# Optimization experiments

Hardware: AMD Instinct MI355X
Metric: run time of the kernel (lower is better)

The kernel has to match this reference:

```python
import jax, jax.numpy as jnp
import numpy as np

V, E, U = 32000, 256, 512  # vocab, embed dim, LSTM units
B, S = 16, 130             # batch, seq len


def lstm_layer(x, mask, k, r, b):
    """Keras LSTMCell semantics. x:[B,T,D], mask:[B,T]; gates order i,f,c,o."""
    h0 = jnp.zeros((x.shape[0], U), x.dtype)
    c0 = h0
    xs = jnp.swapaxes(x, 0, 1)      # [T,B,D]
    ms = jnp.swapaxes(mask, 0, 1)   # [T,B]

    def step(carry, inp):
        h, c = carry
        xt, mt = inp
        z = xt @ k + h @ r + b
        i, f, g, o = jnp.split(z, 4, axis=-1)
        i = jax.nn.sigmoid(i); f = jax.nn.sigmoid(f); o = jax.nn.sigmoid(o)
        cn = f * c + i * jnp.tanh(g)
        hn = o * jnp.tanh(cn)
        m = mt[:, None]
        hn = jnp.where(m, hn, h)  # masked steps carry previous state/output
        cn = jnp.where(m, cn, c)
        return (hn, cn), hn

    _, ys = jax.lax.scan(step, (h0, c0), (xs, ms))
    return jnp.swapaxes(ys, 0, 1)  # [B,T,U]


def stacked_lstm(x, mask, params):
    h = x
    for (k, r, b) in params:
        h = lstm_layer(h, mask, k, r, b)
    return h


def setup_inputs() -> dict:
    key = jax.random.key(0)
    ks = jax.random.split(key, 20)
    d = {}
    d["seqs"] = jax.random.randint(ks[0], (B, S), 0, V)
    d["emb"] = jax.random.normal(ks[1], (V, E), jnp.float32) * 0.01
    i = 2
    for pre in ("f", "b"):
        in_dims = [E, U]
        for l in range(2):
            d[f"{pre}k{l}"] = jax.random.normal(ks[i], (in_dims[l], 4 * U), jnp.float32) * 0.05; i += 1
            d[f"{pre}r{l}"] = jax.random.normal(ks[i], (U, 4 * U), jnp.float32) * 0.05; i += 1
            d[f"{pre}b{l}"] = jnp.zeros((4 * U,), jnp.float32)
    d["Wp"] = jax.random.normal(ks[i], (2 * U, V), jnp.float32) * 0.02
    d["bp"] = jnp.zeros((V,), jnp.float32)
    return d


def reference(seqs, emb, fk0, fr0, fb0, fk1, fr1, fb1, bk0, br0, bb0, bk1, br1, bb1, Wp, bp):
    mask = seqs != 0                 # mask_zero=True
    embedded = emb[seqs]             # [B,S,E]
    # forward LM over tokens 0..S-2
    f = stacked_lstm(embedded[:, :-1], mask[:, :-1], [(fk0, fr0, fb0), (fk1, fr1, fb1)])
    # backward LM over tokens 1..S-1 (go_backwards: scan reversed input)
    xb = embedded[:, 1:][:, ::-1]
    mb = mask[:, 1:][:, ::-1]
    b = stacked_lstm(xb, mb, [(bk0, br0, bb0), (bk1, br1, bb1)])
    b_rev = b[:, ::-1]               # tf.reverse -> chronological order
    o = jnp.concatenate([f[:, :-1], b_rev[:, 1:]], axis=-1)  # [B,S-2,2U]
    return o @ Wp + bp               # [B,S-2,V]
```

## Files before the change

### kernel.cpp

```cpp
#include <hip/hip_runtime.h>

typedef __attribute__((ext_vector_type(8))) short bf16x8;
typedef __attribute__((ext_vector_type(4))) float f32x4;

__device__ __forceinline__ unsigned short f2bf(float x){
  union { float f; unsigned u; } v; v.f = x;
  unsigned r = v.u + 0x7FFFu + ((v.u >> 16) & 1u);
  return (unsigned short)(r >> 16);
}

__device__ __forceinline__ float sigm(float x){
  return 1.f / (1.f + __builtin_amdgcn_exp2f(-1.44269504f * x));
}
__device__ __forceinline__ float tanhfast(float x){
  return 2.f / (1.f + __builtin_amdgcn_exp2f(-2.88539008f * x)) - 1.f;
}

#define BYPASS_ST_SHORT(base, val) \
  asm volatile("global_store_short %0, %1, off sc0 sc1" :: "v"(base), "v"(val))

__device__ __forceinline__ int ld_flag(const int* p){
  int v;
  asm volatile("global_load_dword %0, %1, off sc0 sc1\n\t"
               "s_waitcnt vmcnt(0)"
               : "=v"(v) : "v"(p) : "memory");
  return v;
}

__device__ __forceinline__ void gload_lds16(const void* g, void* l){
  __builtin_amdgcn_global_load_lds(
      (const __attribute__((address_space(1))) unsigned*)g,
      (__attribute__((address_space(3))) unsigned*)l, 16, 0, 0);
}

__global__ void embed_kernel(const int* __restrict__ seqs, const float* __restrict__ emb,
                             unsigned short* __restrict__ x, int* __restrict__ mask,
                             int* __restrict__ flags){
  const int t = blockIdx.x, b = blockIdx.y, l = threadIdx.x;
  if (t == 0 && b == 0){
    #pragma unroll
    for (int j = 0; j < 16; ++j) flags[l + j*64] = 0;
  }
  const int tok = seqs[b*130 + t];
  if (l == 0) mask[b*130 + t] = (tok != 0) ? 1 : 0;
  const float* src = emb + (size_t)tok * 256;
  unsigned short* dst = x + ((size_t)b*130 + t)*256;
  #pragma unroll
  for (int j = 0; j < 4; ++j) dst[l + j*64] = f2bf(src[l + j*64]);
}

__global__ __launch_bounds__(512) void prep_small(
    const float* __restrict__ fk0, unsigned short* __restrict__ fk0T,
    const float* __restrict__ fr0, unsigned short* __restrict__ fr0T,
    const float* __restrict__ fk1, unsigned short* __restrict__ fk1T,
    const float* __restrict__ fr1, unsigned short* __restrict__ fr1T,
    const float* __restrict__ bk0, unsigned short* __restrict__ bk0T,
    const float* __restrict__ br0, unsigned short* __restrict__ br0T,
    const float* __restrict__ bk1, unsigned short* __restrict__ bk1T,
    const float* __restrict__ br1, unsigned short* __restrict__ br1T)
{
  __shared__ float tf[32*65];
  const int tid = threadIdx.x;
  const int tx = tid & 63, ty = tid >> 6;
  const int orow = tid & 31, oc = tid >> 5;
  for (int tile = blockIdx.x; tile < 3584; tile += gridDim.x){
    const float* src; unsigned short* dst; int R, r0, c0;
    int u = tile;
    if (u < 256)      { src = fk0; dst = fk0T; R = 256;           }
    else if (u < 768) { src = fr0; dst = fr0T; R = 512; u -= 256; }
    else if (u < 1280){ src = fk1; dst = fk1T; R = 512; u -= 768; }
    else if (u < 1792){ src = fr1; dst = fr1T; R = 512; u -= 1280;}
    else if (u < 2048){ src = bk0; dst = bk0T; R = 256; u -= 1792;}
    else if (u < 2560){ src = br0; dst = br0T; R = 512; u -= 2048;}
    else if (u < 3072){ src = bk1; dst = bk1T; R = 512; u -= 2560;}
    else              { src = br1; dst = br1T; R = 512; u -= 3072;}
    const int kt = u >> 5, nt = u & 31;
    r0 = kt*32; c0 = nt*64;
    #pragma unroll
    for (int j = 0; j < 4; ++j)
      tf[(ty + 8*j)*65 + tx] = src[(size_t)(r0 + ty + 8*j)*2048 + c0 + tx];
    __syncthreads();
    #pragma unroll
    for (int j = 0; j < 4; ++j)
      dst[(size_t)(c0 + oc + 16*j)*R + r0 + orow] = f2bf(tf[orow*65 + oc + 16*j]);
    __syncthreads();
  }
}

__global__ __launch_bounds__(512, 2) void lstm_coop(
    const unsigned short* __restrict__ x, const int* __restrict__ maskg,
    const unsigned short* __restrict__ fk0T, const unsigned short* __restrict__ fr0T,
    const unsigned short* __restrict__ fk1T, const unsigned short* __restrict__ fr1T,
    const unsigned short* __restrict__ bk0T, const unsigned short* __restrict__ br0T,
    const unsigned short* __restrict__ bk1T, const unsigned short* __restrict__ br1T,
    const float* __restrict__ fb0, const float* __restrict__ fb1,
    const float* __restrict__ bb0, const float* __restrict__ bb1,
    const float* __restrict__ Wp, unsigned short* __restrict__ WpT,
    unsigned short* h0f, unsigned short* h0b,
    unsigned short* aproj, int* flags)
{
  const int wg = blockIdx.x;
  const int tid = threadIdx.x;

  __shared__ float z_lds[4][16][32];
  __shared__ int mask_s[16*130];
  __shared__ __attribute__((aligned(16))) char h_lds[16*1024];
  __shared__ __attribute__((aligned(16))) char h2_lds[16*1024];

  if (wg >= 64){
    float* tf = (float*)h_lds;
    const int tw = wg - 64;
    const int tx = tid & 63, ty = tid >> 6;
    const int orow = tid & 31, oc = tid >> 5;
    for (int tile = tw; tile < 16000; tile += 96){
      const int kt = tile / 500, nt = tile - kt*500;
      const int r0 = kt*32, c0 = nt*64;
      #pragma unroll
      for (int j = 0; j < 4; ++j)
        tf[(ty + 8*j)*65 + tx] = Wp[(size_t)(r0 + ty + 8*j)*32000 + c0 + tx];
      __syncthreads();
      #pragma unroll
      for (int j = 0; j < 4; ++j)
        WpT[(size_t)(c0 + oc + 16*j)*1024 + r0 + orow] = f2bf(tf[orow*65 + oc + 16*j]);
      __syncthreads();
    }
    return;
  }

  const int dir = wg >> 5;
  const int layer = (wg >> 4) & 1;
  const int u0 = (wg & 15) * 32;
  const int w = tid >> 6, l = tid & 63;
  const int gate = w >> 1, half = w & 1;
  const int lr = l & 15, lk = l >> 4;
  const int cglob = gate*512 + u0 + half*16 + lr;

  const unsigned short* kT = (layer == 0) ? (dir ? bk0T : fk0T) : (dir ? bk1T : fk1T);
  const unsigned short* rT = (layer == 0) ? (dir ? br0T : fr0T) : (dir ? br1T : fr1T);
  const float* bias = (layer == 0) ? (dir ? bb0 : fb0) : (dir ? bb1 : fb1);
  unsigned short* h0 = dir ? h0b : h0f;

  int* fown  = flags + (layer*2 + dir)*256;
  int* fprod = flags + dir*256;
  int* fself = fown + (wg & 15)*16;

  bf16x8 wreg[16], kreg[16];
  #pragma unroll
  for (int i = 0; i < 16; ++i)
    wreg[i] = *(const bf16x8*)(rT + (size_t)cglob*512 + i*32 + lk*8);
  if (layer == 0){
    #pragma unroll
    for (int i = 0; i < 8; ++i)
      kreg[i] = *(const bf16x8*)(kT + (size_t)cglob*256 + i*32 + lk*8);
  } else {
    #pragma unroll
    for (int i = 0; i < 16; ++i)
      kreg[i] = *(const bf16x8*)(kT + (size_t)cglob*512 + i*32 + lk*8);
  }

  for (int i = tid; i < 16*130; i += 512) mask_s[i] = maskg[i];

  float c_reg = 0.f, h_reg = 0.f;
  const int gu = tid & 31, gb = tid >> 5;
  const float bzi = bias[u0+gu], bzf = bias[512 + u0+gu];
  const float bzc = bias[1024 + u0+gu], bzo = bias[1536 + u0+gu];
  __syncthreads();

  for (int t = 0; t < 128; ++t){
    {
      const int* fp = nullptr; int tgt = 0;
      if (l < 16){ fp = fown + l*16; tgt = t; }
      else if (l < 32 && layer == 1){ fp = fprod + (l-16)*16; tgt = t + 1; }
      if (fp){
        while (ld_flag(fp) < tgt) __builtin_amdgcn_s_sleep(1);
      }
    }

    const int r0s = w*2;
    if (layer == 0){
      if (t > 0){
        #pragma unroll
        for (int j = 0; j < 2; ++j){
          const int r = r0s + j;
          const unsigned short* g = h0 + ((size_t)(t-1)*16 + r)*512 + ((l ^ (r & 7))*8);
          gload_lds16(g, h_lds + r*1024);
        }
      }
    } else {
      #pragma unroll
      for (int j = 0; j < 2; ++j){
        const int r = r0s + j;
        const unsigned short* g = h0 + ((size_t)t*16 + r)*512 + ((l ^ (r & 7))*8);
        gload_lds16(g, h_lds + r*1024);
      }
      if (t > 0){
        const int prow = dir ? (128 - t) : (t - 1);
        #pragma unroll
        for (int j = 0; j < 2; ++j){
          const int r = r0s + j;
          const unsigned short* g = aproj + ((size_t)(r*128 + prow))*1024 + dir*512 + ((l ^ (r & 7))*8);
          gload_lds16(g, h2_lds + r*1024);
        }
      }
    }

    f32x4 a0 = {0.f,0.f,0.f,0.f}, a1 = a0;
    const int fsw = (lr & 7) << 4;
    if (layer == 0){
      const int pos = dir ? (129 - t) : t;
      const unsigned short* xa = x + ((size_t)lr*130 + pos)*256 + lk*8;
      #pragma unroll
      for (int i = 0; i < 8; i += 2){
        bf16x8 va = *(const bf16x8*)(xa + i*32);
        bf16x8 vb = *(const bf16x8*)(xa + i*32 + 32);
        a0 = __builtin_amdgcn_mfma_f32_16x16x32_bf16(va, kreg[i],   a0, 0, 0, 0);
        a1 = __builtin_amdgcn_mfma_f32_16x16x32_bf16(vb, kreg[i+1], a1, 0, 0, 0);
      }
      if (t > 0){
        asm volatile("s_waitcnt vmcnt(0)" ::: "memory");
        __syncthreads();
        #pragma unroll
        for (int i = 0; i < 16; i += 2){
          bf16x8 v0 = *(const bf16x8*)(h_lds + lr*1024 + ((lk*16 + (i  )*64) ^ fsw));
          bf16x8 v1 = *(const bf16x8*)(h_lds + lr*1024 + ((lk*16 + (i+1)*64) ^ fsw));
          a0 = __builtin_amdgcn_mfma_f32_16x16x32_bf16(v0, wreg[i],   a0, 0, 0, 0);
          a1 = __builtin_amdgcn_mfma_f32_16x16x32_bf16(v1, wreg[i+1], a1, 0, 0, 0);
        }
      }
    } else {
      asm volatile("s_waitcnt vmcnt(0)" ::: "memory");
      __syncthreads();
      #pragma unroll
      for (int i = 0; i < 16; i += 2){
        bf16x8 v0 = *(const bf16x8*)(h_lds + lr*1024 + ((lk*16 + (i  )*64) ^ fsw));
        bf16x8 v1 = *(const bf16x8*)(h_lds + lr*1024 + ((lk*16 + (i+1)*64) ^ fsw));
        a0 = __builtin_amdgcn_mfma_f32_16x16x32_bf16(v0, kreg[i],   a0, 0, 0, 0);
        a1 = __builtin_amdgcn_mfma_f32_16x16x32_bf16(v1, kreg[i+1], a1, 0, 0, 0);
      }
      if (t > 0){
        #pragma unroll
        for (int i = 0; i < 16; i += 2){
          bf16x8 v0 = *(const bf16x8*)(h2_lds + lr*1024 + ((lk*16 + (i  )*64) ^ fsw));
          bf16x8 v1 = *(const bf16x8*)(h2_lds + lr*1024 + ((lk*16 + (i+1)*64) ^ fsw));
          a0 = __builtin_amdgcn_mfma_f32_16x16x32_bf16(v0, wreg[i],   a0, 0, 0, 0);
          a1 = __builtin_amdgcn_mfma_f32_16x16x32_bf16(v1, wreg[i+1], a1, 0, 0, 0);
        }
      }
    }
    {
      f32x4 acc = a0 + a1;
      #pragma unroll
      for (int r = 0; r < 4; ++r) z_lds[gate][lk*4 + r][half*16 + lr] = acc[r];
    }
    __syncthreads();

    {
      const float zi = z_lds[0][gb][gu] + bzi;
      const float zf = z_lds[1][gb][gu] + bzf;
      const float zc = z_lds[2][gb][gu] + bzc;
      const float zo = z_lds[3][gb][gu] + bzo;
      const float iv = sigm(zi);
      const float fv = sigm(zf);
      const float ov = sigm(zo);
      const float gv = tanhfast(zc);
      float cn = fv*c_reg + iv*gv;
      float hn = ov*tanhfast(cn);
      const int pos = dir ? (129 - t) : t;
      if (mask_s[gb*130 + pos] == 0){ cn = c_reg; hn = h_reg; }
      c_reg = cn; h_reg = hn;
      const unsigned short hb = f2bf(hn);
      if (layer == 0){
        unsigned short* p = h0 + ((size_t)t*16 + gb)*512 + u0 + gu;
        BYPASS_ST_SHORT(p, (unsigned)hb);
      } else {
        const int row = dir ? (127 - t) : t;
        unsigned short* p = aproj + ((size_t)gb*128 + row)*1024 + dir*512 + u0 + gu;
        BYPASS_ST_SHORT(p, (unsigned)hb);
      }
    }
    asm volatile("s_waitcnt vmcnt(0)" ::: "memory");
    __syncthreads();
    if (tid == 0){
      int v = t + 1;
      asm volatile("global_store_dword %0, %1, off sc0 sc1" :: "v"(fself), "v"(v) : "memory");
    }
  }
}

__global__ __launch_bounds__(256) void gemm_bf16(
    const unsigned short* __restrict__ A, const unsigned short* __restrict__ Bt,
    const float* __restrict__ bias, float* __restrict__ C,
    int M, int N, int K)
{
  __shared__ unsigned short lA[3][128*32], lB[3][128*32];
  const int tid = threadIdx.x;
  const int w = tid >> 6, l = tid & 63;
  const int wr = w >> 1, wc = w & 1;
  const int lr = l & 15, lk = l >> 4;
  const int orig = blockIdx.x;
  const int logical = (orig & 7)*500 + (orig >> 3);
  const int mt = logical & 15;
  const int nt = logical >> 4;
  const int brow = mt * 128, bcol = nt * 128;

  const int base0 = w*2048;
  const int base1 = w*2048 + 1024;
  const int L0 = base0 + l*16, L1 = base1 + l*16;
  const int Lg0 = L0 ^ (((L0 >> 7) & 3) << 4);
  const int Lg1 = L1 ^ (((L1 >> 7) & 3) << 4);
  const int row0 = Lg0 >> 6, kb0 = Lg0 & 63;
  const int row1 = Lg1 >> 6, kb1 = Lg1 & 63;

  f32x4 acc[4][4] = {};

  #define STAGE_KT(kt_, bu_) do{ \
    const int k0_ = (kt_) * 32; \
    gload_lds16((const char*)(A + (size_t)(brow+row0)*K + k0_) + kb0, (char*)lA[bu_] + base0); \
    gload_lds16((const char*)(Bt + (size_t)(bcol+row0)*K + k0_) + kb0, (char*)lB[bu_] + base0); \
    gload_lds16((const char*)(A + (size_t)(brow+row1)*K + k0_) + kb1, (char*)lA[bu_] + base1); \
    gload_lds16((const char*)(Bt + (size_t)(bcol+row1)*K + k0_) + kb1, (char*)lB[bu_] + base1); \
  }while(0)

  STAGE_KT(0, 0);
  STAGE_KT(1, 1);
  asm volatile("s_waitcnt vmcnt(4)" ::: "memory");
  __syncthreads();

  for (int kt = 0; kt < 32; ++kt){
    const int bu = kt - (kt / 3) * 3;
    if (kt < 30){
      const int nb = (kt + 2) - ((kt + 2) / 3) * 3;
      STAGE_KT(kt + 2, nb);
    }
    bf16x8 af[4], bfr[4];
    #pragma unroll
    for (int m = 0; m < 4; ++m){
      const int L = (wr*64 + m*16 + lr)*64 + lk*16;
      const int sp = L ^ (((L >> 7) & 3) << 4);
      af[m] = *(const bf16x8*)((char*)lA[bu] + sp);
    }
    #pragma unroll
    for (int n = 0; n < 4; ++n){
      const int L = (wc*64 + n*16 + lr)*64 + lk*16;
      const int sp = L ^ (((L >> 7) & 3) << 4);
      bfr[n] = *(const bf16x8*)((char*)lB[bu] + sp);
    }
    #pragma unroll
    for (int m = 0; m < 4; ++m)
      #pragma unroll
      for (int n = 0; n < 4; ++n)
        acc[m][n] = __builtin_amdgcn_mfma_f32_16x16x32_bf16(af[m], bfr[n], acc[m][n], 0, 0, 0);
    if (kt < 31){
      if (kt < 30) asm volatile("s_waitcnt vmcnt(4)" ::: "memory");
      else         asm volatile("s_waitcnt vmcnt(0)" ::: "memory");
      __syncthreads();
    }
  }
  #undef STAGE_KT

  #pragma unroll
  for (int m = 0; m < 4; ++m){
    #pragma unroll
    for (int n = 0; n < 4; ++n){
      const int col = bcol + wc*64 + n*16 + lr;
      const float bv = bias[col];
      const int row0_ = brow + wr*64 + m*16 + lk*4;
      #pragma unroll
      for (int r = 0; r < 4; ++r)
        C[(size_t)(row0_ + r)*N + col] = acc[m][n][r] + bv;
    }
  }
}

extern "C" void kernel_launch(void* const* d_in, const int* in_sizes, int n_in,
                              void* d_out, int out_size, void* d_ws, size_t ws_size,
                              hipStream_t stream){
  (void)in_sizes; (void)n_in; (void)out_size; (void)ws_size;
  const int*   seqs = (const int*)d_in[0];
  const float* emb  = (const float*)d_in[1];
  const float* fk0  = (const float*)d_in[2];
  const float* fr0  = (const float*)d_in[3];
  const float* fb0  = (const float*)d_in[4];
  const float* fk1  = (const float*)d_in[5];
  const float* fr1  = (const float*)d_in[6];
  const float* fb1  = (const float*)d_in[7];
  const float* bk0  = (const float*)d_in[8];
  const float* br0  = (const float*)d_in[9];
  const float* bb0  = (const float*)d_in[10];
  const float* bk1  = (const float*)d_in[11];
  const float* br1  = (const float*)d_in[12];
  const float* bb1  = (const float*)d_in[13];
  const float* Wp   = (const float*)d_in[14];
  const float* bp   = (const float*)d_in[15];
  float* out = (float*)d_out;

  char* ws = (char*)d_ws;
  size_t off = 0;
  auto alloc = [&](size_t b){ size_t o = off; off += (b + 255) & ~(size_t)255; return o; };
  int* flags            = (int*)(ws + alloc(4096));
  unsigned short* x     = (unsigned short*)(ws + alloc((size_t)16*130*256*2));
  int* mask             = (int*)(ws + alloc((size_t)16*130*4));
  unsigned short* fk0T  = (unsigned short*)(ws + alloc((size_t)2048*256*2));
  unsigned short* fr0T  = (unsigned short*)(ws + alloc((size_t)2048*512*2));
  unsigned short* fk1T  = (unsigned short*)(ws + alloc((size_t)2048*512*2));
  unsigned short* fr1T  = (unsigned short*)(ws + alloc((size_t)2048*512*2));
  unsigned short* bk0T  = (unsigned short*)(ws + alloc((size_t)2048*256*2));
  unsigned short* br0T  = (unsigned short*)(ws + alloc((size_t)2048*512*2));
  unsigned short* bk1T  = (unsigned short*)(ws + alloc((size_t)2048*512*2));
  unsigned short* br1T  = (unsigned short*)(ws + alloc((size_t)2048*512*2));
  unsigned short* h0f   = (unsigned short*)(ws + alloc((size_t)128*16*512*2));
  unsigned short* h0b   = (unsigned short*)(ws + alloc((size_t)128*16*512*2));
  unsigned short* aproj = (unsigned short*)(ws + alloc((size_t)2048*1024*2));
  unsigned short* WpT   = (unsigned short*)(ws + alloc((size_t)32000*1024*2));

  embed_kernel<<<dim3(130,16), 64, 0, stream>>>(seqs, emb, x, mask, flags);

  prep_small<<<256, 512, 0, stream>>>(
      fk0, fk0T, fr0, fr0T, fk1, fk1T, fr1, fr1T,
      bk0, bk0T, br0, br0T, bk1, bk1T, br1, br1T);

  lstm_coop<<<160, 512, 0, stream>>>(x, mask,
      fk0T, fr0T, fk1T, fr1T, bk0T, br0T, bk1T, br1T,
      fb0, fb1, bb0, bb1, Wp, WpT, h0f, h0b, aproj, flags);

  gemm_bf16<<<4000, 256, 0, stream>>>(aproj, WpT, bp, out, 2048, 32000, 1024);
}
```

Before: 799.7 us.

## Retile projection GEMM to 256x256 blocks and merge embed/prep kernels

The output-projection GEMM moves from 128x128 tiles (256 threads, K-step 32, triple buffer) to 256x256 tiles with 512 threads, K-step 64, a double-buffered LDS pipeline and a wider XOR swizzle. This raises operand reuse per block and interleaves the next-stage loads with the MFMA phases. The cost is 128KB of LDS per block, so only one block fits per CU, plus a full vmcnt(0) wait and barrier every iteration. Separately, the embedding gather and the weight transpose/convert kernels are merged into one launch to save a kernel launch.

```diff
diff --git a/kernel.cpp b/kernel.cpp
--- a/kernel.cpp
+++ b/kernel.cpp
@@ -33,23 +33,9 @@
       (__attribute__((address_space(3))) unsigned*)l, 16, 0, 0);
 }
 
-__global__ void embed_kernel(const int* __restrict__ seqs, const float* __restrict__ emb,
-                             unsigned short* __restrict__ x, int* __restrict__ mask,
-                             int* __restrict__ flags){
-  const int t = blockIdx.x, b = blockIdx.y, l = threadIdx.x;
-  if (t == 0 && b == 0){
-    #pragma unroll
-    for (int j = 0; j < 16; ++j) flags[l + j*64] = 0;
-  }
-  const int tok = seqs[b*130 + t];
-  if (l == 0) mask[b*130 + t] = (tok != 0) ? 1 : 0;
-  const float* src = emb + (size_t)tok * 256;
-  unsigned short* dst = x + ((size_t)b*130 + t)*256;
-  #pragma unroll
-  for (int j = 0; j < 4; ++j) dst[l + j*64] = f2bf(src[l + j*64]);
-}
-
-__global__ __launch_bounds__(512) void prep_small(
+__global__ __launch_bounds__(512) void embed_prep(
+    const int* __restrict__ seqs, const float* __restrict__ emb,
+    unsigned short* __restrict__ x, int* __restrict__ mask, int* __restrict__ flags,
     const float* __restrict__ fk0, unsigned short* __restrict__ fk0T,
     const float* __restrict__ fr0, unsigned short* __restrict__ fr0T,
     const float* __restrict__ fk1, unsigned short* __restrict__ fk1T,
@@ -60,11 +46,27 @@
     const float* __restrict__ br1, unsigned short* __restrict__ br1T)
 {
   __shared__ float tf[32*65];
-  const int tid = threadIdx.x;
+  const int blk = blockIdx.x, tid = threadIdx.x;
+  if (blk < 260){
+    if (blk == 0 && tid < 64){
+      #pragma unroll
+      for (int j = 0; j < 16; ++j) flags[tid + j*64] = 0;
+    }
+    const int idx = blk*8 + (tid >> 6);
+    const int lane = tid & 63;
+    const int b = idx / 130, t = idx - b*130;
+    const int tok = seqs[b*130 + t];
+    if (lane == 0) mask[b*130 + t] = (tok != 0) ? 1 : 0;
+    const float* src = emb + (size_t)tok * 256;
+    unsigned short* dst = x + ((size_t)b*130 + t)*256;
+    #pragma unroll
+    for (int j = 0; j < 4; ++j) dst[lane + j*64] = f2bf(src[lane + j*64]);
+    return;
+  }
   const int tx = tid & 63, ty = tid >> 6;
   const int orow = tid & 31, oc = tid >> 5;
-  for (int tile = blockIdx.x; tile < 3584; tile += gridDim.x){
-    const float* src; unsigned short* dst; int R, r0, c0;
+  for (int tile = blk - 260; tile < 3584; tile += 256){
+    const float* src; unsigned short* dst; int R;
     int u = tile;
     if (u < 256)      { src = fk0; dst = fk0T; R = 256;           }
     else if (u < 768) { src = fr0; dst = fr0T; R = 512; u -= 256; }
@@ -75,7 +77,7 @@
     else if (u < 3072){ src = bk1; dst = bk1T; R = 512; u -= 2560;}
     else              { src = br1; dst = br1T; R = 512; u -= 3072;}
     const int kt = u >> 5, nt = u & 31;
-    r0 = kt*32; c0 = nt*64;
+    const int r0 = kt*32, c0 = nt*64;
     #pragma unroll
     for (int j = 0; j < 4; ++j)
       tf[(ty + 8*j)*65 + tx] = src[(size_t)(r0 + ty + 8*j)*2048 + c0 + tx];
@@ -287,87 +289,79 @@
   }
 }
 
-__global__ __launch_bounds__(256) void gemm_bf16(
+#define SWZ7(L) ((L) ^ ((((L) >> 7) & 7) << 4))
+__global__ __launch_bounds__(512) void gemm_bf16(
     const unsigned short* __restrict__ A, const unsigned short* __restrict__ Bt,
     const float* __restrict__ bias, float* __restrict__ C,
     int M, int N, int K)
 {
-  __shared__ unsigned short lA[3][128*32], lB[3][128*32];
+  __shared__ unsigned short lA[2][256*64], lB[2][256*64];
   const int tid = threadIdx.x;
   const int w = tid >> 6, l = tid & 63;
-  const int wr = w >> 1, wc = w & 1;
+  const int wm = w >> 2, wn = w & 3;
   const int lr = l & 15, lk = l >> 4;
   const int orig = blockIdx.x;
-  const int logical = (orig & 7)*500 + (orig >> 3);
-  const int mt = logical & 15;
-  const int nt = logical >> 4;
-  const int brow = mt * 128, bcol = nt * 128;
-
-  const int base0 = w*2048;
-  const int base1 = w*2048 + 1024;
-  const int L0 = base0 + l*16, L1 = base1 + l*16;
-  const int Lg0 = L0 ^ (((L0 >> 7) & 3) << 4);
-  const int Lg1 = L1 ^ (((L1 >> 7) & 3) << 4);
-  const int row0 = Lg0 >> 6, kb0 = Lg0 & 63;
-  const int row1 = Lg1 >> 6, kb1 = Lg1 & 63;
-
-  f32x4 acc[4][4] = {};
-
-  #define STAGE_KT(kt_, bu_) do{ \
-    const int k0_ = (kt_) * 32; \
-    gload_lds16((const char*)(A + (size_t)(brow+row0)*K + k0_) + kb0, (char*)lA[bu_] + base0); \
-    gload_lds16((const char*)(Bt + (size_t)(bcol+row0)*K + k0_) + kb0, (char*)lB[bu_] + base0); \
-    gload_lds16((const char*)(A + (size_t)(brow+row1)*K + k0_) + kb1, (char*)lA[bu_] + base1); \
-    gload_lds16((const char*)(Bt + (size_t)(bcol+row1)*K + k0_) + kb1, (char*)lB[bu_] + base1); \
+  const int logical = (orig & 7)*125 + (orig >> 3);
+  const int mt = logical & 7;
+  const int nt = logical >> 3;
+  const int brow = mt*256, bcol = nt*256;
+
+  f32x4 acc[8][4] = {};
+
+  #define STG(kt_, s_, j_) do{ \
+    const int Lw = w*4096 + (j_)*1024 + l*16; \
+    const int Lg = SWZ7(Lw); \
+    const int rw = Lg >> 7, cb = Lg & 127; \
+    gload_lds16((const char*)(A + (size_t)(brow+rw)*K + (kt_)*64) + cb, \
+                (char*)lA[s_] + w*4096 + (j_)*1024); \
+    gload_lds16((const char*)(Bt + (size_t)(bcol+rw)*K + (kt_)*64) + cb, \
+                (char*)lB[s_] + w*4096 + (j_)*1024); \
   }while(0)
 
-  STAGE_KT(0, 0);
-  STAGE_KT(1, 1);
-  asm volatile("s_waitcnt vmcnt(4)" ::: "memory");
+  #pragma unroll
+  for (int j = 0; j < 4; ++j) STG(0, 0, j);
+  asm volatile("s_waitcnt vmcnt(0)" ::: "memory");
   __syncthreads();
 
-  for (int kt = 0; kt < 32; ++kt){
-    const int bu = kt - (kt / 3) * 3;
-    if (kt < 30){
-      const int nb = (kt + 2) - ((kt + 2) / 3) * 3;
-      STAGE_KT(kt + 2, nb);
-    }
-    bf16x8 af[4], bfr[4];
-    #pragma unroll
-    for (int m = 0; m < 4; ++m){
-      const int L = (wr*64 + m*16 + lr)*64 + lk*16;
-      const int sp = L ^ (((L >> 7) & 3) << 4);
-      af[m] = *(const bf16x8*)((char*)lA[bu] + sp);
-    }
+  for (int kt = 0; kt < 16; ++kt){
+    const int s = kt & 1;
+    #pragma unroll
+    for (int p = 0; p < 4; ++p){
+      if (kt < 15) STG(kt + 1, s ^ 1, p);
+      const int ks = p >> 1, mh = p & 1;
+      bf16x8 bf[4], af[4];
+      #pragma unroll
+      for (int n = 0; n < 4; ++n){
+        const int L = (wn*64 + n*16 + lr)*128 + ks*64 + lk*16;
+        bf[n] = *(const bf16x8*)((const char*)lB[s] + SWZ7(L));
+      }
+      #pragma unroll
+      for (int m4 = 0; m4 < 4; ++m4){
+        const int L = (wm*128 + (mh*4 + m4)*16 + lr)*128 + ks*64 + lk*16;
+        af[m4] = *(const bf16x8*)((const char*)lA[s] + SWZ7(L));
+      }
+      #pragma unroll
+      for (int m4 = 0; m4 < 4; ++m4)
+        #pragma unroll
+        for (int n = 0; n < 4; ++n)
+          acc[mh*4 + m4][n] = __builtin_amdgcn_mfma_f32_16x16x32_bf16(
+              af[m4], bf[n], acc[mh*4 + m4][n], 0, 0, 0);
+    }
+    asm volatile("s_waitcnt vmcnt(0)" ::: "memory");
+    __syncthreads();
+  }
+  #undef STG
+
+  #pragma unroll
+  for (int m = 0; m < 8; ++m){
     #pragma unroll
     for (int n = 0; n < 4; ++n){
-      const int L = (wc*64 + n*16 + lr)*64 + lk*16;
-      const int sp = L ^ (((L >> 7) & 3) << 4);
-      bfr[n] = *(const bf16x8*)((char*)lB[bu] + sp);
-    }
-    #pragma unroll
-    for (int m = 0; m < 4; ++m)
-      #pragma unroll
-      for (int n = 0; n < 4; ++n)
-        acc[m][n] = __builtin_amdgcn_mfma_f32_16x16x32_bf16(af[m], bfr[n], acc[m][n], 0, 0, 0);
-    if (kt < 31){
-      if (kt < 30) asm volatile("s_waitcnt vmcnt(4)" ::: "memory");
-      else         asm volatile("s_waitcnt vmcnt(0)" ::: "memory");
-      __syncthreads();
-    }
-  }
-  #undef STAGE_KT
-
-  #pragma unroll
-  for (int m = 0; m < 4; ++m){
-    #pragma unroll
-    for (int n = 0; n < 4; ++n){
-      const int col = bcol + wc*64 + n*16 + lr;
+      const int col = bcol + wn*64 + n*16 + lr;
       const float bv = bias[col];
-      const int row0_ = brow + wr*64 + m*16 + lk*4;
+      const int r0 = brow + wm*128 + m*16 + lk*4;
       #pragma unroll
       for (int r = 0; r < 4; ++r)
-        C[(size_t)(row0_ + r)*N + col] = acc[m][n][r] + bv;
+        C[(size_t)(r0 + r)*N + col] = acc[m][n][r] + bv;
     }
   }
 }
@@ -413,9 +407,7 @@
   unsigned short* aproj = (unsigned short*)(ws + alloc((size_t)2048*1024*2));
   unsigned short* WpT   = (unsigned short*)(ws + alloc((size_t)32000*1024*2));
 
-  embed_kernel<<<dim3(130,16), 64, 0, stream>>>(seqs, emb, x, mask, flags);
-
-  prep_small<<<256, 512, 0, stream>>>(
+  embed_prep<<<516, 512, 0, stream>>>(seqs, emb, x, mask, flags,
       fk0, fk0T, fr0, fr0T, fk1, fk1T, fr1, fr1T,
       bk0, bk0T, br0, br0T, bk1, bk1T, br1, br1T);
 
@@ -423,5 +415,5 @@
       fk0T, fr0T, fk1T, fr1T, bk0T, br0T, bk1T, br1T,
       fb0, fb1, bb0, bb1, Wp, WpT, h0f, h0b, aproj, flags);
 
-  gemm_bf16<<<4000, 256, 0, stream>>>(aproj, WpT, bp, out, 2048, 32000, 1024);
-}
+  gemm_bf16<<<1000, 512, 0, stream>>>(aproj, WpT, bp, out, 2048, 32000, 1024);
+}
```

Result: no change. 805.4 us (+0.7%).
